# Performance work log

Hardware: AMD Instinct MI355X
Metric: run time of the kernel (lower is better)

Reference implementation:

```python
import jax, jax.numpy as jnp
import numpy as np


def setup_inputs() -> dict:
    key = jax.random.key(0)
    ks = jax.random.split(key, 10)
    B, L, H, E, D = 2, 2048, 16, 64, 64
    d_model = 512
    inp = {
        "queries": jax.random.normal(ks[0], (B, L, H, E), jnp.float32),
        "keys": jax.random.normal(ks[1], (B, L, H, E), jnp.float32),
        "values": jax.random.normal(ks[2], (B, L, H, D), jnp.float32),
        "raw_series": jax.random.normal(ks[3], (B, L, d_model), jnp.float32),
        # learned fusion MLP: Linear(d_model, d_model//2) -> ReLU -> Linear(d_model//2, 1)
        "w1": jax.random.normal(ks[4], (d_model, d_model // 2), jnp.float32) / np.sqrt(d_model),
        "b1": jnp.zeros((d_model // 2,), jnp.float32),
        "w2": jax.random.normal(ks[5], (d_model // 2, 1), jnp.float32) / np.sqrt(d_model // 2),
        "b2": jnp.zeros((1,), jnp.float32),
        # per-head trend scaling, init ones
        "alpha_trend": jnp.ones((H,), jnp.float32),
    }
    return inp


MOMENTUM_ALPHA = 1.0
MOMENTUM_K = 1


def reference(queries, keys, values, raw_series, w1, b1, w2, b2, alpha_trend):
    B, L, H, E = queries.shape
    scale = 1.0 / jnp.sqrt(jnp.asarray(E, queries.dtype))

    # ---- soft momentum bias ----
    # learned fusion: MLP over features -> scalar per position, [B, L]
    h = jax.nn.relu(raw_series @ w1 + b1)
    fused = (h @ w2 + b2)[..., 0]                       # [B, L]
    k = max(1, min(MOMENTUM_K, L - 1))
    momentum = fused[:, k:] - fused[:, :-k]              # [B, L-k]
    momentum = jnp.pad(momentum, ((0, 0), (k, 0)))       # left-pad zeros -> [B, L]
    diff = jnp.abs(momentum[:, :, None] - momentum[:, None, :])  # [B, L, L]
    soft_bias = -MOMENTUM_ALPHA * diff                   # [B, L, L]

    # ---- attention ----
    scores = jnp.einsum('blhe,bshe->bhls', queries, keys)  # [B, H, L, L]
    scores = scores + soft_bias[:, None, :, :] * alpha_trend[None, :, None, None]
    causal = jnp.triu(jnp.ones((L, L), bool), k=1)       # True above diagonal
    scores = jnp.where(causal[None, None], -jnp.inf, scores)
    A = jax.nn.softmax(scale * scores, axis=-1)          # [B, H, L, L]
    V = jnp.einsum('bhls,bshd->blhd', A, values)         # [B, L, H, D]
    return V
```

## Files before the change

### kernel.cpp

```cpp
#include <hip/hip_runtime.h>
#include <math.h>

#define B_ 2
#define L_ 2048
#define H_ 16
#define E_ 64
#define D_ 64
#define DM_ 512
#define DH_ 256

typedef __bf16 bf16_t;
typedef bf16_t bf16x8_t __attribute__((ext_vector_type(8)));
typedef float f32x4_t __attribute__((ext_vector_type(4)));

__device__ __forceinline__ unsigned bpack(float hi, float lo) {
    unsigned uh = __float_as_uint(hi) + 0x8000u;
    unsigned ul = __float_as_uint(lo) + 0x8000u;
    return __builtin_amdgcn_perm(uh, ul, 0x07060302u);
}

__device__ __forceinline__ bf16_t to_bf16(float f) {
    union { float f; unsigned u; } x; x.f = f;
    unsigned r = (x.u + 0x7fffu + ((x.u >> 16) & 1u)) >> 16;
    union { unsigned short s; bf16_t b; } y; y.s = (unsigned short)r;
    return y.b;
}

__global__ __launch_bounds__(256) void transpose_w1_kernel(
        const float* __restrict__ w1, bf16_t* __restrict__ w1t) {
    __shared__ float sT[64][65];
    const int t  = threadIdx.x;
    const int k0 = (blockIdx.x >> 2) * 64;
    const int n0 = (blockIdx.x & 3) * 64;
    const int nn = t & 63;
    #pragma unroll
    for (int u = 0; u < 16; ++u) {
        int k = (t >> 6) + u * 4;
        sT[k][nn] = w1[(size_t)(k0 + k) * DH_ + n0 + nn];
    }
    __syncthreads();
    const int nr = t >> 2;
    const int kc = (t & 3) * 16;
    unsigned pk0[8];
    #pragma unroll
    for (int j = 0; j < 8; ++j)
        pk0[j] = bpack(sT[kc + 2 * j + 1][nr], sT[kc + 2 * j][nr]);
    bf16_t* dst = w1t + (size_t)(n0 + nr) * DM_ + k0 + kc;
    ((uint2*)dst)[0] = make_uint2(pk0[0], pk0[1]);
    ((uint2*)dst)[1] = make_uint2(pk0[2], pk0[3]);
    ((uint2*)dst)[2] = make_uint2(pk0[4], pk0[5]);
    ((uint2*)dst)[3] = make_uint2(pk0[6], pk0[7]);
}

__global__ __launch_bounds__(256) void mlp_kernel(
        const float* __restrict__ raw, const bf16_t* __restrict__ w1t,
        const float* __restrict__ b1, const float* __restrict__ w2,
        float* __restrict__ fused) {
    __shared__ bf16_t Rs[16][520];
    __shared__ float pk[2][4][16][17];
    __shared__ float part[2][16];
    const int t  = threadIdx.x;
    const int m0 = (blockIdx.x >> 1) * 16;
    const int nh = blockIdx.x & 1;
    #pragma unroll
    for (int u = 0; u < 8; ++u) {
        int idx = t + u * 256;
        int row = idx >> 7;
        int k   = (idx & 127) << 2;
        f32x4_t v = *(const f32x4_t*)&raw[(size_t)(m0 + row) * DM_ + k];
        uint2 p;
        p.x = bpack(v[1], v[0]);
        p.y = bpack(v[3], v[2]);
        *(uint2*)&Rs[row][k] = p;
    }
    __syncthreads();
    const int wave = t >> 6;
    const int lane = t & 63;
    const int lrow = lane & 15;
    const int lgrp = lane >> 4;
    const int kh   = wave >> 1;
    const int nq   = wave & 1;
    const int n0w  = nh * 128 + nq * 64;
    const int k0   = kh * 256;

    f32x4_t acc[4];
    #pragma unroll
    for (int nt = 0; nt < 4; ++nt) acc[nt] = (f32x4_t){0.f, 0.f, 0.f, 0.f};

    const bf16_t* wbase = w1t + (size_t)(n0w + lrow) * DM_ + k0 + lgrp * 8;
    #pragma unroll
    for (int s = 0; s < 8; ++s) {
        bf16x8_t a = *(const bf16x8_t*)&Rs[lrow][k0 + s * 32 + lgrp * 8];
        #pragma unroll
        for (int nt = 0; nt < 4; ++nt) {
            bf16x8_t b = *(const bf16x8_t*)(wbase + nt * 16 * DM_ + s * 32);
            acc[nt] = __builtin_amdgcn_mfma_f32_16x16x32_bf16(a, b, acc[nt], 0, 0, 0);
        }
    }
    if (kh == 1) {
        #pragma unroll
        for (int nt = 0; nt < 4; ++nt)
            #pragma unroll
            for (int r = 0; r < 4; ++r)
                pk[nq][nt][lgrp * 4 + r][lrow] = acc[nt][r];
    }
    __syncthreads();
    if (kh == 0) {
        float rowpart[4] = {0.f, 0.f, 0.f, 0.f};
        #pragma unroll
        for (int nt = 0; nt < 4; ++nt) {
            int n = n0w + nt * 16 + lrow;
            float b1v = b1[n];
            float w2v = w2[n];
            #pragma unroll
            for (int r = 0; r < 4; ++r) {
                float hv = acc[nt][r] + pk[nq][nt][lgrp * 4 + r][lrow] + b1v;
                hv = hv > 0.f ? hv : 0.f;
                rowpart[r] += hv * w2v;
            }
        }
        #pragma unroll
        for (int r = 0; r < 4; ++r) {
            float v = rowpart[r];
            v += __shfl_xor(v, 1);
            v += __shfl_xor(v, 2);
            v += __shfl_xor(v, 4);
            v += __shfl_xor(v, 8);
            if (lrow == 0) part[nq][lgrp * 4 + r] = v;
        }
    }
    __syncthreads();
    if (t < 16)
        atomicAdd(&fused[m0 + t], part[0][t] + part[1][t]);
}

__global__ __launch_bounds__(128, 3) void attn_kernel(
        const float* __restrict__ Q, const float* __restrict__ K,
        const float* __restrict__ V, const float* __restrict__ fused,
        const float* __restrict__ alpha_trend, float* __restrict__ out,
        bf16_t* __restrict__ pO, float* __restrict__ prs) {
    __shared__ bf16_t Ks[64][72];
    __shared__ bf16_t Vt[64][76];
    __shared__ unsigned short Ps[2][32][68];
    __shared__ float moms[64];

    const int bid  = blockIdx.x;
    const int bh   = bid & 31;
    const int wid  = bid >> 5;
    int qt, sa, sb, chunk;
    bool split;
    if (wid < 32) {
        qt    = 31 - (wid >> 1);
        chunk = wid & 1;
        int half = (qt + 2) >> 1;
        sa = chunk ? half : 0;
        sb = chunk ? qt + 1 : half;
        split = true;
    } else {
        qt = 47 - wid;
        sa = 0; sb = qt + 1; chunk = 0;
        split = false;
    }
    const int h    = bh & 15;
    const int b    = bh >> 4;
    const int q0   = qt << 6;
    const int tid  = threadIdx.x;
    const int wave = tid >> 6;
    const int lane = tid & 63;
    const int lrow = lane & 15;
    const int lgrp = lane >> 4;

    const float c1      = 0.18033688f;
    const float ascale2 = alpha_trend[h] * c1;
    const size_t bl     = (size_t)b * L_;
    const int qw0       = q0 + wave * 32;

    const float* Kb = K + (bl * H_ + h) * E_;
    const float* Vb = V + (bl * H_ + h) * D_;
    const float* fp = fused + bl;

    const int krow = tid >> 4;
    const int ke0  = (tid & 15) << 2;
    const int vd   = tid & 63;
    const int vsb  = tid >> 6;

    bf16x8_t aq[2][2];
    #pragma unroll
    for (int mh = 0; mh < 2; ++mh) {
        const float* qp = Q + ((bl + qw0 + mh * 16 + lrow) * H_ + h) * E_ + lgrp * 8;
        f32x4_t v0 = *(const f32x4_t*)(qp);
        f32x4_t v1 = *(const f32x4_t*)(qp + 4);
        f32x4_t v2 = *(const f32x4_t*)(qp + 32);
        f32x4_t v3 = *(const f32x4_t*)(qp + 36);
        #pragma unroll
        for (int k = 0; k < 4; ++k) {
            aq[mh][0][k]     = to_bf16(v0[k] * c1);
            aq[mh][0][4 + k] = to_bf16(v1[k] * c1);
            aq[mh][1][k]     = to_bf16(v2[k] * c1);
            aq[mh][1][4 + k] = to_bf16(v3[k] * c1);
        }
    }
    float mq[2][4];
    #pragma unroll
    for (int mh = 0; mh < 2; ++mh)
        #pragma unroll
        for (int r = 0; r < 4; ++r) {
            int l = qw0 + mh * 16 + lgrp * 4 + r;
            mq[mh][r] = (l == 0) ? 0.f : fp[l] - fp[l - 1];
        }

    f32x4_t Oacc[2][4];
    #pragma unroll
    for (int mh = 0; mh < 2; ++mh)
        #pragma unroll
        for (int c = 0; c < 4; ++c) Oacc[mh][c] = (f32x4_t){0.f, 0.f, 0.f, 0.f};
    float rowsum[2][4] = {{0.f, 0.f, 0.f, 0.f}, {0.f, 0.f, 0.f, 0.f}};

    for (int st = sa; st < sb; ++st) {
        const int s0 = st << 6;
        __syncthreads();
        #pragma unroll
        for (int u = 0; u < 8; ++u) {
            int srow = krow + u * 8;
            f32x4_t kv = *(const f32x4_t*)&Kb[(s0 + srow) * (H_ * E_) + ke0];
            uint2 p;
            p.x = bpack(kv[1], kv[0]);
            p.y = bpack(kv[3], kv[2]);
            *(uint2*)&Ks[srow][ke0] = p;
        }
        float vv[32];
        #pragma unroll
        for (int j = 0; j < 32; ++j)
            vv[j] = Vb[(s0 + vsb * 32 + j) * (H_ * D_) + vd];
        #pragma unroll
        for (int u = 0; u < 8; ++u) {
            uint2 p;
            p.x = bpack(vv[u * 4 + 1], vv[u * 4 + 0]);
            p.y = bpack(vv[u * 4 + 3], vv[u * 4 + 2]);
            *(uint2*)&Vt[vd][vsb * 32 + u * 4] = p;
        }
        if (tid < 64) {
            int l_ = s0 + tid;
            moms[tid] = (l_ == 0) ? 0.f : fp[l_] - fp[l_ - 1];
        }
        __syncthreads();

        f32x4_t Sacc[2][4];
        #pragma unroll
        for (int mh = 0; mh < 2; ++mh)
            #pragma unroll
            for (int c = 0; c < 4; ++c) Sacc[mh][c] = (f32x4_t){0.f, 0.f, 0.f, 0.f};
        #pragma unroll
        for (int c = 0; c < 4; ++c) {
            bf16x8_t b_lo = *(const bf16x8_t*)&Ks[c * 16 + lrow][lgrp * 8];
            bf16x8_t b_hi = *(const bf16x8_t*)&Ks[c * 16 + lrow][32 + lgrp * 8];
            #pragma unroll
            for (int mh = 0; mh < 2; ++mh) {
                Sacc[mh][c] = __builtin_amdgcn_mfma_f32_16x16x32_bf16(aq[mh][0], b_lo, Sacc[mh][c], 0, 0, 0);
                Sacc[mh][c] = __builtin_amdgcn_mfma_f32_16x16x32_bf16(aq[mh][1], b_hi, Sacc[mh][c], 0, 0, 0);
            }
        }

        unsigned short* Psw = &Ps[wave][0][0];
        #pragma unroll
        for (int c = 0; c < 4; ++c) {
            float ms = moms[c * 16 + lrow];
            int sg = s0 + c * 16 + lrow;
            #pragma unroll
            for (int mh = 0; mh < 2; ++mh) {
                #pragma unroll
                for (int r = 0; r < 4; ++r) {
                    float arg = Sacc[mh][c][r] - ascale2 * fabsf(mq[mh][r] - ms);
                    float e = __builtin_amdgcn_exp2f(arg);
                    if (st == qt && sg > qw0 + mh * 16 + lgrp * 4 + r) e = 0.f;
                    Psw[(mh * 16 + lgrp * 4 + r) * 68 + c * 16 + lrow] =
                        (unsigned short)(__float_as_uint(e) >> 16);
                    rowsum[mh][r] += e;
                }
            }
        }

        #pragma unroll
        for (int hh = 0; hh < 2; ++hh) {
            union { uint2 u2[2]; bf16x8_t v; } ap[2];
            #pragma unroll
            for (int mh = 0; mh < 2; ++mh) {
                ap[mh].u2[0] = *(const uint2*)&Psw[(mh * 16 + lrow) * 68 + hh * 32 + lgrp * 8];
                ap[mh].u2[1] = *(const uint2*)&Psw[(mh * 16 + lrow) * 68 + hh * 32 + lgrp * 8 + 4];
            }
            #pragma unroll
            for (int c2 = 0; c2 < 4; ++c2) {
                union { uint2 u2[2]; bf16x8_t v; } bb;
                bb.u2[0] = *(const uint2*)&Vt[c2 * 16 + lrow][hh * 32 + lgrp * 8];
                bb.u2[1] = *(const uint2*)&Vt[c2 * 16 + lrow][hh * 32 + lgrp * 8 + 4];
                #pragma unroll
                for (int mh = 0; mh < 2; ++mh)
                    Oacc[mh][c2] = __builtin_amdgcn_mfma_f32_16x16x32_bf16(ap[mh].v, bb.v, Oacc[mh][c2], 0, 0, 0);
            }
        }
    }

    #pragma unroll
    for (int mh = 0; mh < 2; ++mh) {
        #pragma unroll
        for (int r = 0; r < 4; ++r) {
            float rs = rowsum[mh][r];
            rs += __shfl_xor(rs, 1);
            rs += __shfl_xor(rs, 2);
            rs += __shfl_xor(rs, 4);
            rs += __shfl_xor(rs, 8);
            if (!split) {
                float inv = 1.f / rs;
                size_t orow = ((bl + qw0 + mh * 16 + lgrp * 4 + r) * H_ + h) * D_;
                #pragma unroll
                for (int c = 0; c < 4; ++c)
                    out[orow + c * 16 + lrow] = Oacc[mh][c][r] * inv;
            } else {
                const int slot = (bh * 16 + (qt - 16)) * 2 + chunk;
                bf16_t* po = pO + (size_t)slot * 4096;
                float*  pr = prs + (size_t)slot * 64;
                int q = wave * 32 + mh * 16 + lgrp * 4 + r;
                if (lrow == 0) pr[q] = rs;
                #pragma unroll
                for (int c = 0; c < 4; ++c)
                    po[q * 64 + c * 16 + lrow] = to_bf16(Oacc[mh][c][r]);
            }
        }
    }
}

__global__ __launch_bounds__(256) void merge_kernel(
        const bf16_t* __restrict__ pO, const float* __restrict__ prs,
        float* __restrict__ out) {
    const int bid = blockIdx.x;
    const int bh  = bid & 31;
    const int qt  = 16 + (bid >> 5);
    const int h   = bh & 15;
    const int b   = bh >> 4;
    const int t   = threadIdx.x;
    const int q   = t >> 2;
    const int d0  = (t & 3) << 4;

    const int slotA = (bh * 16 + (qt - 16)) * 2;
    const bf16_t* poA = pO + (size_t)slotA * 4096 + q * 64 + d0;
    const bf16_t* poB = poA + 4096;
    float rs = prs[slotA * 64 + q] + prs[(slotA + 1) * 64 + q];
    float inv = 1.f / rs;

    float* op = out + (((size_t)b * L_ + (qt << 6) + q) * H_ + h) * D_ + d0;
    #pragma unroll
    for (int i = 0; i < 16; i += 4) {
        f32x4_t o;
        #pragma unroll
        for (int k = 0; k < 4; ++k)
            o[k] = ((float)poA[i + k] + (float)poB[i + k]) * inv;
        *(f32x4_t*)&op[i] = o;
    }
}

extern "C" void kernel_launch(void* const* d_in, const int* in_sizes, int n_in,
                              void* d_out, int out_size, void* d_ws, size_t ws_size,
                              hipStream_t stream) {
    const float* Q     = (const float*)d_in[0];
    const float* K     = (const float*)d_in[1];
    const float* V     = (const float*)d_in[2];
    const float* raw   = (const float*)d_in[3];
    const float* w1    = (const float*)d_in[4];
    const float* b1    = (const float*)d_in[5];
    const float* w2    = (const float*)d_in[6];
    const float* alpha = (const float*)d_in[8];
    float* out = (float*)d_out;

    float* fused = (float*)d_ws;
    bf16_t* w1t  = (bf16_t*)(fused + B_ * L_);
    bf16_t* pO   = w1t + (size_t)DH_ * DM_;
    float* prs   = (float*)(pO + (size_t)1024 * 4096);

    hipMemsetAsync(fused, 0, B_ * L_ * sizeof(float), stream);
    transpose_w1_kernel<<<32, 256, 0, stream>>>(w1, w1t);
    mlp_kernel<<<B_ * L_ / 16 * 2, 256, 0, stream>>>(raw, w1t, b1, w2, fused);
    attn_kernel<<<1536, 128, 0, stream>>>(Q, K, V, fused, alpha, out, pO, prs);
    merge_kernel<<<512, 256, 0, stream>>>(pO, prs, out);
}
```

Measured before the change: 173.4 us.

## Drop w1 transpose and memset; register-prefetch next K/V tile in attention

New measurement: 248.5 us. 1.43x slower.

```diff
diff --git a/kernel.cpp b/kernel.cpp
--- a/kernel.cpp
+++ b/kernel.cpp
@@ -26,42 +26,15 @@
     return y.b;
 }
 
-__global__ __launch_bounds__(256) void transpose_w1_kernel(
-        const float* __restrict__ w1, bf16_t* __restrict__ w1t) {
-    __shared__ float sT[64][65];
-    const int t  = threadIdx.x;
-    const int k0 = (blockIdx.x >> 2) * 64;
-    const int n0 = (blockIdx.x & 3) * 64;
-    const int nn = t & 63;
-    #pragma unroll
-    for (int u = 0; u < 16; ++u) {
-        int k = (t >> 6) + u * 4;
-        sT[k][nn] = w1[(size_t)(k0 + k) * DH_ + n0 + nn];
-    }
-    __syncthreads();
-    const int nr = t >> 2;
-    const int kc = (t & 3) * 16;
-    unsigned pk0[8];
-    #pragma unroll
-    for (int j = 0; j < 8; ++j)
-        pk0[j] = bpack(sT[kc + 2 * j + 1][nr], sT[kc + 2 * j][nr]);
-    bf16_t* dst = w1t + (size_t)(n0 + nr) * DM_ + k0 + kc;
-    ((uint2*)dst)[0] = make_uint2(pk0[0], pk0[1]);
-    ((uint2*)dst)[1] = make_uint2(pk0[2], pk0[3]);
-    ((uint2*)dst)[2] = make_uint2(pk0[4], pk0[5]);
-    ((uint2*)dst)[3] = make_uint2(pk0[6], pk0[7]);
-}
-
 __global__ __launch_bounds__(256) void mlp_kernel(
-        const float* __restrict__ raw, const bf16_t* __restrict__ w1t,
+        const float* __restrict__ raw, const float* __restrict__ w1,
         const float* __restrict__ b1, const float* __restrict__ w2,
         float* __restrict__ fused) {
     __shared__ bf16_t Rs[16][520];
-    __shared__ float pk[2][4][16][17];
+    __shared__ float pk[2][8][16][17];
     __shared__ float part[2][16];
     const int t  = threadIdx.x;
-    const int m0 = (blockIdx.x >> 1) * 16;
-    const int nh = blockIdx.x & 1;
+    const int m0 = blockIdx.x * 16;
     #pragma unroll
     for (int u = 0; u < 8; ++u) {
         int idx = t + u * 256;
@@ -80,26 +53,34 @@
     const int lgrp = lane >> 4;
     const int kh   = wave >> 1;
     const int nq   = wave & 1;
-    const int n0w  = nh * 128 + nq * 64;
     const int k0   = kh * 256;
-
-    f32x4_t acc[4];
-    #pragma unroll
-    for (int nt = 0; nt < 4; ++nt) acc[nt] = (f32x4_t){0.f, 0.f, 0.f, 0.f};
-
-    const bf16_t* wbase = w1t + (size_t)(n0w + lrow) * DM_ + k0 + lgrp * 8;
+    const int n0   = nq * 128;
+
+    f32x4_t acc[8];
+    #pragma unroll
+    for (int nt = 0; nt < 8; ++nt) acc[nt] = (f32x4_t){0.f, 0.f, 0.f, 0.f};
+
     #pragma unroll
     for (int s = 0; s < 8; ++s) {
-        bf16x8_t a = *(const bf16x8_t*)&Rs[lrow][k0 + s * 32 + lgrp * 8];
-        #pragma unroll
-        for (int nt = 0; nt < 4; ++nt) {
-            bf16x8_t b = *(const bf16x8_t*)(wbase + nt * 16 * DM_ + s * 32);
-            acc[nt] = __builtin_amdgcn_mfma_f32_16x16x32_bf16(a, b, acc[nt], 0, 0, 0);
+        const int kbase = k0 + s * 32 + lgrp * 8;
+        bf16x8_t a = *(const bf16x8_t*)&Rs[lrow][kbase];
+        const float* wp = w1 + (size_t)kbase * DH_ + n0 + lrow;
+        #pragma unroll
+        for (int nt = 0; nt < 8; ++nt) {
+            float f[8];
+            #pragma unroll
+            for (int j = 0; j < 8; ++j) f[j] = wp[j * DH_ + nt * 16];
+            union { uint2 u2[2]; bf16x8_t v; } bb;
+            bb.u2[0].x = bpack(f[1], f[0]);
+            bb.u2[0].y = bpack(f[3], f[2]);
+            bb.u2[1].x = bpack(f[5], f[4]);
+            bb.u2[1].y = bpack(f[7], f[6]);
+            acc[nt] = __builtin_amdgcn_mfma_f32_16x16x32_bf16(a, bb.v, acc[nt], 0, 0, 0);
         }
     }
     if (kh == 1) {
         #pragma unroll
-        for (int nt = 0; nt < 4; ++nt)
+        for (int nt = 0; nt < 8; ++nt)
             #pragma unroll
             for (int r = 0; r < 4; ++r)
                 pk[nq][nt][lgrp * 4 + r][lrow] = acc[nt][r];
@@ -108,8 +89,8 @@
     if (kh == 0) {
         float rowpart[4] = {0.f, 0.f, 0.f, 0.f};
         #pragma unroll
-        for (int nt = 0; nt < 4; ++nt) {
-            int n = n0w + nt * 16 + lrow;
+        for (int nt = 0; nt < 8; ++nt) {
+            int n = n0 + nt * 16 + lrow;
             float b1v = b1[n];
             float w2v = w2[n];
             #pragma unroll
@@ -131,8 +112,10 @@
     }
     __syncthreads();
     if (t < 16)
-        atomicAdd(&fused[m0 + t], part[0][t] + part[1][t]);
-}
+        fused[m0 + t] = part[0][t] + part[1][t];
+}
+
+struct TileRegs { f32x4_t k[8]; float v[32]; float m; };
 
 __global__ __launch_bounds__(128, 3) void attn_kernel(
         const float* __restrict__ Q, const float* __restrict__ K,
@@ -216,34 +199,44 @@
         for (int c = 0; c < 4; ++c) Oacc[mh][c] = (f32x4_t){0.f, 0.f, 0.f, 0.f};
     float rowsum[2][4] = {{0.f, 0.f, 0.f, 0.f}, {0.f, 0.f, 0.f, 0.f}};
 
+    TileRegs tr;
+    #define LOAD_TILE(st_) do {                                                   \
+        const int s0_ = (st_) << 6;                                               \
+        _Pragma("unroll")                                                         \
+        for (int u = 0; u < 8; ++u)                                               \
+            tr.k[u] = *(const f32x4_t*)&Kb[(s0_ + krow + u * 8) * (H_ * E_) + ke0]; \
+        _Pragma("unroll")                                                         \
+        for (int j = 0; j < 32; ++j)                                              \
+            tr.v[j] = Vb[(s0_ + vsb * 32 + j) * (H_ * D_) + vd];                  \
+        if (tid < 64) {                                                           \
+            int l_ = s0_ + tid;                                                   \
+            tr.m = (l_ == 0) ? 0.f : fp[l_] - fp[l_ - 1];                         \
+        }                                                                         \
+    } while (0)
+
+    LOAD_TILE(sa);
+
     for (int st = sa; st < sb; ++st) {
         const int s0 = st << 6;
         __syncthreads();
         #pragma unroll
         for (int u = 0; u < 8; ++u) {
-            int srow = krow + u * 8;
-            f32x4_t kv = *(const f32x4_t*)&Kb[(s0 + srow) * (H_ * E_) + ke0];
             uint2 p;
-            p.x = bpack(kv[1], kv[0]);
-            p.y = bpack(kv[3], kv[2]);
-            *(uint2*)&Ks[srow][ke0] = p;
-        }
-        float vv[32];
-        #pragma unroll
-        for (int j = 0; j < 32; ++j)
-            vv[j] = Vb[(s0 + vsb * 32 + j) * (H_ * D_) + vd];
+            p.x = bpack(tr.k[u][1], tr.k[u][0]);
+            p.y = bpack(tr.k[u][3], tr.k[u][2]);
+            *(uint2*)&Ks[krow + u * 8][ke0] = p;
+        }
         #pragma unroll
         for (int u = 0; u < 8; ++u) {
             uint2 p;
-            p.x = bpack(vv[u * 4 + 1], vv[u * 4 + 0]);
-            p.y = bpack(vv[u * 4 + 3], vv[u * 4 + 2]);
+            p.x = bpack(tr.v[u * 4 + 1], tr.v[u * 4 + 0]);
+            p.y = bpack(tr.v[u * 4 + 3], tr.v[u * 4 + 2]);
             *(uint2*)&Vt[vd][vsb * 32 + u * 4] = p;
         }
-        if (tid < 64) {
-            int l_ = s0 + tid;
-            moms[tid] = (l_ == 0) ? 0.f : fp[l_] - fp[l_ - 1];
-        }
+        if (tid < 64) moms[tid] = tr.m;
         __syncthreads();
+
+        if (st + 1 < sb) LOAD_TILE(st + 1);
 
         f32x4_t Sacc[2][4];
         #pragma unroll
@@ -327,6 +320,7 @@
             }
         }
     }
+    #undef LOAD_TILE
 }
 
 __global__ __launch_bounds__(256) void merge_kernel(
@@ -372,13 +366,10 @@
     float* out = (float*)d_out;
 
     float* fused = (float*)d_ws;
-    bf16_t* w1t  = (bf16_t*)(fused + B_ * L_);
-    bf16_t* pO   = w1t + (size_t)DH_ * DM_;
+    bf16_t* pO   = (bf16_t*)(fused + B_ * L_);
     float* prs   = (float*)(pO + (size_t)1024 * 4096);
 
-    hipMemsetAsync(fused, 0, B_ * L_ * sizeof(float), stream);
-    transpose_w1_kernel<<<32, 256, 0, stream>>>(w1, w1t);
-    mlp_kernel<<<B_ * L_ / 16 * 2, 256, 0, stream>>>(raw, w1t, b1, w2, fused);
+    mlp_kernel<<<B_ * L_ / 16, 256, 0, stream>>>(raw, w1, b1, w2, fused);
     attn_kernel<<<1536, 128, 0, stream>>>(Q, K, V, fused, alpha, out, pO, prs);
     merge_kernel<<<512, 256, 0, stream>>>(pO, prs, out);
 }
```
